# Performance work log

Hardware: AMD Instinct MI355X
Metric: run time of the kernel (lower is better)

## Reference

```python
import jax, jax.numpy as jnp
import numpy as np

BATCH = 65536
IN_DIM = 512
LATENT = 32
NUM_TRIL = LATENT * (LATENT + 1) // 2  # 528
# torch.tril_indices returns row-major order, same as np.tril_indices
_ROWS, _COLS = np.tril_indices(LATENT)
ROWS = jnp.asarray(_ROWS)
COLS = jnp.asarray(_COLS)
BN_EPS = 1e-5
LRELU_SLOPE = 0.01


def setup_inputs() -> dict:
    key = jax.random.key(0)
    ks = jax.random.split(key, 12)
    x = jax.random.normal(ks[0], (BATCH, IN_DIM), dtype=jnp.float32)
    s_enc = 1.0 / np.sqrt(IN_DIM)
    s_lat = 1.0 / np.sqrt(LATENT)
    return {
        "x": x,
        "W_enc": jax.random.uniform(ks[1], (IN_DIM, LATENT), minval=-s_enc, maxval=s_enc, dtype=jnp.float32),
        "b_enc": jax.random.uniform(ks[2], (LATENT,), minval=-s_enc, maxval=s_enc, dtype=jnp.float32),
        "bn_gamma": jnp.ones((LATENT,), dtype=jnp.float32),
        "bn_beta": jnp.zeros((LATENT,), dtype=jnp.float32),
        "bn_mean": 0.1 * jax.random.normal(ks[3], (LATENT,), dtype=jnp.float32),
        "bn_var": jax.random.uniform(ks[4], (LATENT,), minval=0.5, maxval=1.5, dtype=jnp.float32),
        "W_mu": jax.random.uniform(ks[5], (LATENT, LATENT), minval=-s_lat, maxval=s_lat, dtype=jnp.float32),
        "b_mu": jax.random.uniform(ks[6], (LATENT,), minval=-s_lat, maxval=s_lat, dtype=jnp.float32),
        "W_ch": jax.random.uniform(ks[7], (LATENT, NUM_TRIL), minval=-s_lat, maxval=s_lat, dtype=jnp.float32),
        "b_ch": jax.random.uniform(ks[8], (NUM_TRIL,), minval=-s_lat, maxval=s_lat, dtype=jnp.float32),
    }


def _leaky_relu(v):
    return jnp.where(v >= 0, v, LRELU_SLOPE * v)


def reference(x, W_enc, b_enc, bn_gamma, bn_beta, bn_mean, bn_var, W_mu, b_mu, W_ch, b_ch):
    # downsampled_enc: Linear(512, latent) -> BatchNorm1d (eval mode) -> LeakyReLU
    h = x @ W_enc + b_enc                                        # [B, L]
    h = bn_gamma * (h - bn_mean) * jax.lax.rsqrt(bn_var + BN_EPS) + bn_beta
    h = _leaky_relu(h)
    # mu head
    mus = _leaky_relu(h @ W_mu + b_mu)                           # [B, L]
    # log-cholesky head -> 528 lower-triangular elements
    elts = _leaky_relu(h @ W_ch + b_ch)                          # [B, 528]
    B = x.shape[0]
    L = jnp.zeros((B, LATENT, LATENT), dtype=jnp.float32)
    L = L.at[:, ROWS, COLS].set(elts)                            # scatter into lower triangle
    di = jnp.arange(LATENT)
    diag = L[:, di, di]
    diag = jnp.clip(jax.nn.softplus(diag), 0.001, 100.0) + 0.01
    L = L.at[:, di, di].set(diag)
    # cov = L L^T + 0.01 I
    cov = jnp.einsum('bij,bkj->bik', L, L) + 0.01 * jnp.eye(LATENT, dtype=jnp.float32)
    return (h, mus, cov)
```

## Files before the change

### kernel.cpp

```cpp
#include <hip/hip_runtime.h>
#include <math.h>

constexpr int BATCH  = 65536;
constexpr int IN_DIM = 512;
constexpr int LATENT = 32;
constexpr int NTRIL  = 528;
constexpr float BN_EPS = 1e-5f;
constexpr float SLOPE  = 0.01f;

constexpr int RPB  = 64;
constexpr int CROWS = 16;
constexpr int HSTR = 36;
constexpr int PSTR = 36;

constexpr int LPACK   = 576;
constexpr int LSTRIDE = 584;

__device__ __host__ __forceinline__ constexpr int rstart(int i) {
    const int g = i >> 2, r = i & 3;
    return 4 * (i + 2 * g * (g - 1) + r * g);
}

__device__ __forceinline__ float leaky(float v) {
    return v >= 0.0f ? v : SLOPE * v;
}

extern "C" __global__ __launch_bounds__(256, 4)
void enc_kernel(const float* __restrict__ x,
                const float* __restrict__ W_enc,
                const float* __restrict__ b_enc,
                const float* __restrict__ bn_gamma,
                const float* __restrict__ bn_beta,
                const float* __restrict__ bn_mean,
                const float* __restrict__ bn_var,
                float* __restrict__ h_out)
{
    __shared__ float part[4][RPB][PSTR];

    const int t = threadIdx.x;
    const int w = __builtin_amdgcn_readfirstlane(t >> 6);
    const int l = t & 63;
    const int row0 = blockIdx.x * RPB;

    {
        const float4* __restrict__ xp =
            (const float4*)(x + (size_t)(row0 + l) * IN_DIM + w * (IN_DIM / 4));
        const float* __restrict__ Wq = W_enc + (w * (IN_DIM / 4)) * LATENT;

        float acc[LATENT];
        #pragma unroll
        for (int c = 0; c < LATENT; ++c) acc[c] = 0.0f;

        float4 q0 = xp[0];
        float4 q1 = xp[1];
        #pragma unroll 2
        for (int k4 = 0; k4 < IN_DIM / 16; ++k4) {
            const float4 xv = q0;
            q0 = q1;
            const int pf = (k4 < IN_DIM / 16 - 2) ? (k4 + 2) : (IN_DIM / 16 - 1);
            q1 = xp[pf];

            const float* __restrict__ Wk = Wq + (4 * k4) * LATENT;
            #pragma unroll
            for (int c = 0; c < LATENT; ++c) acc[c] = fmaf(xv.x, Wk[c],            acc[c]);
            #pragma unroll
            for (int c = 0; c < LATENT; ++c) acc[c] = fmaf(xv.y, Wk[LATENT + c],   acc[c]);
            #pragma unroll
            for (int c = 0; c < LATENT; ++c) acc[c] = fmaf(xv.z, Wk[2*LATENT + c], acc[c]);
            #pragma unroll
            for (int c = 0; c < LATENT; ++c) acc[c] = fmaf(xv.w, Wk[3*LATENT + c], acc[c]);
        }

        #pragma unroll
        for (int c4 = 0; c4 < LATENT / 4; ++c4)
            *(float4*)&part[w][l][4 * c4] =
                make_float4(acc[4*c4+0], acc[4*c4+1], acc[4*c4+2], acc[4*c4+3]);
    }
    __syncthreads();

    {
        const int r  = t >> 2;
        const int c0 = (t & 3) * 8;
        float v[8];
        #pragma unroll
        for (int i = 0; i < 8; ++i) v[i] = 0.0f;
        #pragma unroll
        for (int ww = 0; ww < 4; ++ww) {
            const float4 p0 = *(const float4*)&part[ww][r][c0];
            const float4 p1 = *(const float4*)&part[ww][r][c0 + 4];
            v[0]+=p0.x; v[1]+=p0.y; v[2]+=p0.z; v[3]+=p0.w;
            v[4]+=p1.x; v[5]+=p1.y; v[6]+=p1.z; v[7]+=p1.w;
        }
        float hv[8];
        #pragma unroll
        for (int i = 0; i < 8; ++i) {
            const int c = c0 + i;
            float u = v[i] + b_enc[c];
            u = bn_gamma[c] * (u - bn_mean[c]) * rsqrtf(bn_var[c] + BN_EPS) + bn_beta[c];
            hv[i] = leaky(u);
        }
        float4* __restrict__ hp = (float4*)(h_out + (size_t)(row0 + r) * LATENT + c0);
        hp[0] = make_float4(hv[0], hv[1], hv[2], hv[3]);
        hp[1] = make_float4(hv[4], hv[5], hv[6], hv[7]);
    }
}

extern "C" __global__ __launch_bounds__(256)
void elts_kernel(const float* __restrict__ h_in,
                 const float* __restrict__ W_mu,
                 const float* __restrict__ b_mu,
                 const float* __restrict__ W_ch,
                 const float* __restrict__ b_ch,
                 float* __restrict__ mu_out,
                 float* __restrict__ cov_out)
{
    __shared__ float h_sh[RPB][HSTR];

    const int t = threadIdx.x;
    const int row0 = blockIdx.x * RPB;

    {
        const int r  = t >> 2;
        const int c0 = (t & 3) * 8;
        const float4* __restrict__ hg =
            (const float4*)(h_in + (size_t)(row0 + r) * LATENT + c0);
        const float4 a0 = hg[0];
        const float4 a1 = hg[1];
        *(float4*)&h_sh[r][c0]     = a0;
        *(float4*)&h_sh[r][c0 + 4] = a1;
    }
    __syncthreads();

    {
        const int c = t & 31;
        const int g = t >> 5;
        float wmu[LATENT];
        #pragma unroll
        for (int k = 0; k < LATENT; ++k) wmu[k] = W_mu[k * LATENT + c];
        const float bm = b_mu[c];
        #pragma unroll
        for (int j = 0; j < 8; ++j) {
            const int r = g * 8 + j;
            const float4* __restrict__ hr = (const float4*)&h_sh[r][0];
            float a = bm;
            #pragma unroll
            for (int k4 = 0; k4 < 8; ++k4) {
                const float4 hvv = hr[k4];
                a += hvv.x*wmu[4*k4+0] + hvv.y*wmu[4*k4+1]
                   + hvv.z*wmu[4*k4+2] + hvv.w*wmu[4*k4+3];
            }
            mu_out[(size_t)(row0 + r) * LATENT + c] = leaky(a);
        }
    }

    #pragma unroll 1
    for (int jid = t; jid < 132 * 16; jid += 256) {
        const int q  = jid % 132;
        const int rg = jid / 132;
        const int j0 = 4 * q;
        const int r0s = 4 * rg;

        float4 a0 = make_float4(b_ch[j0+0], b_ch[j0+1], b_ch[j0+2], b_ch[j0+3]);
        float4 a1 = a0, a2 = a0, a3 = a0;

        const float* __restrict__ wbase = W_ch + j0;
        #pragma unroll
        for (int kq = 0; kq < 8; ++kq) {
            const float4 w0 = *(const float4*)(wbase + (4*kq + 0) * NTRIL);
            const float4 w1 = *(const float4*)(wbase + (4*kq + 1) * NTRIL);
            const float4 w2 = *(const float4*)(wbase + (4*kq + 2) * NTRIL);
            const float4 w3 = *(const float4*)(wbase + (4*kq + 3) * NTRIL);
            const float4 h0 = *(const float4*)&h_sh[r0s + 0][4*kq];
            const float4 h1 = *(const float4*)&h_sh[r0s + 1][4*kq];
            const float4 h2 = *(const float4*)&h_sh[r0s + 2][4*kq];
            const float4 h3 = *(const float4*)&h_sh[r0s + 3][4*kq];
            a0.x += h0.x*w0.x + h0.y*w1.x + h0.z*w2.x + h0.w*w3.x;
            a0.y += h0.x*w0.y + h0.y*w1.y + h0.z*w2.y + h0.w*w3.y;
            a0.z += h0.x*w0.z + h0.y*w1.z + h0.z*w2.z + h0.w*w3.z;
            a0.w += h0.x*w0.w + h0.y*w1.w + h0.z*w2.w + h0.w*w3.w;
            a1.x += h1.x*w0.x + h1.y*w1.x + h1.z*w2.x + h1.w*w3.x;
            a1.y += h1.x*w0.y + h1.y*w1.y + h1.z*w2.y + h1.w*w3.y;
            a1.z += h1.x*w0.z + h1.y*w1.z + h1.z*w2.z + h1.w*w3.z;
            a1.w += h1.x*w0.w + h1.y*w1.w + h1.z*w2.w + h1.w*w3.w;
            a2.x += h2.x*w0.x + h2.y*w1.x + h2.z*w2.x + h2.w*w3.x;
            a2.y += h2.x*w0.y + h2.y*w1.y + h2.z*w2.y + h2.w*w3.y;
            a2.z += h2.x*w0.z + h2.y*w1.z + h2.z*w2.z + h2.w*w3.z;
            a2.w += h2.x*w0.w + h2.y*w1.w + h2.z*w2.w + h2.w*w3.w;
            a3.x += h3.x*w0.x + h3.y*w1.x + h3.z*w2.x + h3.w*w3.x;
            a3.y += h3.x*w0.y + h3.y*w1.y + h3.z*w2.y + h3.w*w3.y;
            a3.z += h3.x*w0.z + h3.y*w1.z + h3.z*w2.z + h3.w*w3.z;
            a3.w += h3.x*w0.w + h3.y*w1.w + h3.z*w2.w + h3.w*w3.w;
        }

        #pragma unroll
        for (int e = 0; e < 4; ++e) {
            const int j = j0 + e;
            int ri = (int)((sqrtf(8.0f * (float)j + 1.0f) - 1.0f) * 0.5f);
            if ((ri + 1) * (ri + 2) / 2 <= j) ++ri;
            if (ri * (ri + 1) / 2 > j) --ri;
            const int ci = j - ri * (ri + 1) / 2;
            const bool isdiag = (ci == ri);
            const int off = rstart(ri) + ci;

            #pragma unroll
            for (int rr = 0; rr < 4; ++rr) {
                float vv = (rr == 0) ? ((e==0)?a0.x:(e==1)?a0.y:(e==2)?a0.z:a0.w)
                         : (rr == 1) ? ((e==0)?a1.x:(e==1)?a1.y:(e==2)?a1.z:a1.w)
                         : (rr == 2) ? ((e==0)?a2.x:(e==1)?a2.y:(e==2)?a2.z:a2.w)
                                     : ((e==0)?a3.x:(e==1)?a3.y:(e==2)?a3.z:a3.w);
                vv = leaky(vv);
                if (isdiag) {
                    float sp = vv > 20.0f ? vv : log1pf(__expf(vv));
                    vv = fminf(fmaxf(sp, 0.001f), 100.0f) + 0.01f;
                }
                cov_out[(size_t)(row0 + r0s + rr) * (LATENT * LATENT) + off] = vv;
            }
        }
    }
}

extern "C" __global__ __launch_bounds__(256)
void cov_kernel(float* __restrict__ cov_out)
{
    __shared__ float L_sh[CROWS * LSTRIDE];

    const int t = threadIdx.x;
    const int row0b = blockIdx.x * CROWS;

    #pragma unroll 1
    for (int s = t; s < CROWS * (LPACK / 4); s += 256) {
        const int lr = s / (LPACK / 4);
        const int qi = s % (LPACK / 4);
        const float4 v = *(const float4*)
            (cov_out + (size_t)(row0b + lr) * (LATENT * LATENT) + 4 * qi);
        *(float4*)&L_sh[lr * LSTRIDE + 4 * qi] = v;
    }
    __syncthreads();

    #pragma unroll 1
    for (int s = t; s < CROWS * 48; s += 256) {
        const int lr  = s / 48;
        const int idx = s % 48;
        const int g  = idx / 6;
        const int wv = idx % 6;
        const int rig = (wv < 3) ? 0 : (wv < 5) ? 1 : 2;
        const int po  = (wv < 3) ? wv : (wv < 5) ? wv - 3 : 0;
        const int i   = 4 * g + rig;
        L_sh[lr * LSTRIDE + rstart(i) + (i + 1) + po] = 0.0f;
    }
    __syncthreads();

    {
        const int lr = t >> 4;
        const int p  = t & 15;
        const float* __restrict__ Lb = L_sh + lr * LSTRIDE;

        float li0[16];
        {
            const int s0 = rstart(p);
            #pragma unroll
            for (int qq = 0; qq < 4; ++qq) {
                const float4 v = *(const float4*)(Lb + s0 + 4*qq);
                li0[4*qq+0] = (4*qq+0 <= p) ? v.x : 0.0f;
                li0[4*qq+1] = (4*qq+1 <= p) ? v.y : 0.0f;
                li0[4*qq+2] = (4*qq+2 <= p) ? v.z : 0.0f;
                li0[4*qq+3] = (4*qq+3 <= p) ? v.w : 0.0f;
            }
        }
        float li1[32];
        {
            const int i1 = p + 16;
            const int s1 = rstart(i1);
            #pragma unroll
            for (int qq = 0; qq < 8; ++qq) {
                const float4 v = *(const float4*)(Lb + s1 + 4*qq);
                li1[4*qq+0] = (4*qq+0 <= i1) ? v.x : 0.0f;
                li1[4*qq+1] = (4*qq+1 <= i1) ? v.y : 0.0f;
                li1[4*qq+2] = (4*qq+2 <= i1) ? v.z : 0.0f;
                li1[4*qq+3] = (4*qq+3 <= i1) ? v.w : 0.0f;
            }
        }

        float* __restrict__ cov0 =
            cov_out + (size_t)(row0b + lr) * (LATENT * LATENT) + (size_t)p * LATENT;
        float* __restrict__ cov1 = cov0 + 16 * LATENT;

        float cr0[16], cr1[16];

        #pragma unroll
        for (int k = 0; k < 16; ++k) {
            const int qk = (k >> 2) + 1;
            const float* __restrict__ Lk = Lb + rstart(k);
            float d0 = 0.0f, d1 = 0.0f;
            #pragma unroll
            for (int qq = 0; qq < qk; ++qq) {
                const float4 wv = *(const float4*)(Lk + 4*qq);
                d0 += li0[4*qq+0]*wv.x + li0[4*qq+1]*wv.y
                    + li0[4*qq+2]*wv.z + li0[4*qq+3]*wv.w;
                d1 += li1[4*qq+0]*wv.x + li1[4*qq+1]*wv.y
                    + li1[4*qq+2]*wv.z + li1[4*qq+3]*wv.w;
            }
            cr0[k] = (k == p) ? d0 + 0.01f : d0;
            cr1[k] = d1;
        }
        #pragma unroll
        for (int k4 = 0; k4 < 4; ++k4) {
            *(float4*)(cov0 + 4*k4) = make_float4(cr0[4*k4], cr0[4*k4+1], cr0[4*k4+2], cr0[4*k4+3]);
            *(float4*)(cov1 + 4*k4) = make_float4(cr1[4*k4], cr1[4*k4+1], cr1[4*k4+2], cr1[4*k4+3]);
        }

        #pragma unroll
        for (int k = 16; k < 32; ++k) {
            const int qk = (k >> 2) + 1;
            const float* __restrict__ Lk = Lb + rstart(k);
            float d0 = 0.0f, d1 = 0.0f;
            #pragma unroll
            for (int qq = 0; qq < 4; ++qq) {
                const float4 wv = *(const float4*)(Lk + 4*qq);
                d0 += li0[4*qq+0]*wv.x + li0[4*qq+1]*wv.y
                    + li0[4*qq+2]*wv.z + li0[4*qq+3]*wv.w;
            }
            #pragma unroll
            for (int qq = 0; qq < 8; ++qq) {
                if (qq < qk) {
                    const float4 wv = *(const float4*)(Lk + 4*qq);
                    d1 += li1[4*qq+0]*wv.x + li1[4*qq+1]*wv.y
                        + li1[4*qq+2]*wv.z + li1[4*qq+3]*wv.w;
                }
            }
            cr0[k-16] = d0;
            cr1[k-16] = (k == p + 16) ? d1 + 0.01f : d1;
        }
        #pragma unroll
        for (int k4 = 0; k4 < 4; ++k4) {
            *(float4*)(cov0 + 16 + 4*k4) = make_float4(cr0[4*k4], cr0[4*k4+1], cr0[4*k4+2], cr0[4*k4+3]);
            *(float4*)(cov1 + 16 + 4*k4) = make_float4(cr1[4*k4], cr1[4*k4+1], cr1[4*k4+2], cr1[4*k4+3]);
        }
    }
}

extern "C" void kernel_launch(void* const* d_in, const int* in_sizes, int n_in,
                              void* d_out, int out_size, void* d_ws, size_t ws_size,
                              hipStream_t stream) {
    const float* x        = (const float*)d_in[0];
    const float* W_enc    = (const float*)d_in[1];
    const float* b_enc    = (const float*)d_in[2];
    const float* bn_gamma = (const float*)d_in[3];
    const float* bn_beta  = (const float*)d_in[4];
    const float* bn_mean  = (const float*)d_in[5];
    const float* bn_var   = (const float*)d_in[6];
    const float* W_mu     = (const float*)d_in[7];
    const float* b_mu     = (const float*)d_in[8];
    const float* W_ch     = (const float*)d_in[9];
    const float* b_ch     = (const float*)d_in[10];
    float* out = (float*)d_out;

    float* h_out   = out;
    float* mu_out  = out + (size_t)BATCH * LATENT;
    float* cov_out = out + (size_t)2 * BATCH * LATENT;

    enc_kernel<<<dim3(BATCH / RPB), dim3(256), 0, stream>>>(
        x, W_enc, b_enc, bn_gamma, bn_beta, bn_mean, bn_var, h_out);
    elts_kernel<<<dim3(BATCH / RPB), dim3(256), 0, stream>>>(
        h_out, W_mu, b_mu, W_ch, b_ch, mu_out, cov_out);
    cov_kernel<<<dim3(BATCH / CROWS), dim3(256), 0, stream>>>(cov_out);
}
```

Baseline: 807.1 us.

## Fuse Cholesky element and covariance kernels through shared-memory L tiles

The elts and cov kernels are merged into one decoder kernel. The packed lower-triangular L elements are now written to a zeroed shared-memory buffer in sub-blocks of 16 rows instead of going to global memory. The L L^T product is then computed straight from shared memory. This removes the global write and re-read of the packed L (about 2.3 KB per row), one kernel launch and the separate zeroing pass. In exchange it adds about 37 KB of shared memory per block plus extra barriers, which may limit occupancy. The triangular index decode is also made incremental instead of using a per-element sqrt.

```diff
diff --git a/kernel.cpp b/kernel.cpp
--- a/kernel.cpp
+++ b/kernel.cpp
@@ -9,11 +9,10 @@
 constexpr float SLOPE  = 0.01f;
 
 constexpr int RPB  = 64;
-constexpr int CROWS = 16;
+constexpr int SUBR = 16;
 constexpr int HSTR = 36;
 constexpr int PSTR = 36;
 
-constexpr int LPACK   = 576;
 constexpr int LSTRIDE = 584;
 
 __device__ __host__ __forceinline__ constexpr int rstart(int i) {
@@ -105,19 +104,27 @@
     }
 }
 
-extern "C" __global__ __launch_bounds__(256)
-void elts_kernel(const float* __restrict__ h_in,
-                 const float* __restrict__ W_mu,
-                 const float* __restrict__ b_mu,
-                 const float* __restrict__ W_ch,
-                 const float* __restrict__ b_ch,
-                 float* __restrict__ mu_out,
-                 float* __restrict__ cov_out)
+extern "C" __global__ __launch_bounds__(256, 4)
+void dec_kernel(const float* __restrict__ h_in,
+                const float* __restrict__ W_mu,
+                const float* __restrict__ b_mu,
+                const float* __restrict__ W_ch,
+                const float* __restrict__ b_ch,
+                float* __restrict__ mu_out,
+                float* __restrict__ cov_out)
 {
     __shared__ float h_sh[RPB][HSTR];
+    __shared__ float L_sh[SUBR * LSTRIDE];
 
     const int t = threadIdx.x;
     const int row0 = blockIdx.x * RPB;
+
+    {
+        float4* z4 = (float4*)L_sh;
+        const float4 z = make_float4(0.f, 0.f, 0.f, 0.f);
+        #pragma unroll 1
+        for (int s = t; s < SUBR * LSTRIDE / 4; s += 256) z4[s] = z;
+    }
 
     {
         const int r  = t >> 2;
@@ -154,188 +161,164 @@
     }
 
     #pragma unroll 1
-    for (int jid = t; jid < 132 * 16; jid += 256) {
-        const int q  = jid % 132;
-        const int rg = jid / 132;
-        const int j0 = 4 * q;
-        const int r0s = 4 * rg;
-
-        float4 a0 = make_float4(b_ch[j0+0], b_ch[j0+1], b_ch[j0+2], b_ch[j0+3]);
-        float4 a1 = a0, a2 = a0, a3 = a0;
-
-        const float* __restrict__ wbase = W_ch + j0;
-        #pragma unroll
-        for (int kq = 0; kq < 8; ++kq) {
-            const float4 w0 = *(const float4*)(wbase + (4*kq + 0) * NTRIL);
-            const float4 w1 = *(const float4*)(wbase + (4*kq + 1) * NTRIL);
-            const float4 w2 = *(const float4*)(wbase + (4*kq + 2) * NTRIL);
-            const float4 w3 = *(const float4*)(wbase + (4*kq + 3) * NTRIL);
-            const float4 h0 = *(const float4*)&h_sh[r0s + 0][4*kq];
-            const float4 h1 = *(const float4*)&h_sh[r0s + 1][4*kq];
-            const float4 h2 = *(const float4*)&h_sh[r0s + 2][4*kq];
-            const float4 h3 = *(const float4*)&h_sh[r0s + 3][4*kq];
-            a0.x += h0.x*w0.x + h0.y*w1.x + h0.z*w2.x + h0.w*w3.x;
-            a0.y += h0.x*w0.y + h0.y*w1.y + h0.z*w2.y + h0.w*w3.y;
-            a0.z += h0.x*w0.z + h0.y*w1.z + h0.z*w2.z + h0.w*w3.z;
-            a0.w += h0.x*w0.w + h0.y*w1.w + h0.z*w2.w + h0.w*w3.w;
-            a1.x += h1.x*w0.x + h1.y*w1.x + h1.z*w2.x + h1.w*w3.x;
-            a1.y += h1.x*w0.y + h1.y*w1.y + h1.z*w2.y + h1.w*w3.y;
-            a1.z += h1.x*w0.z + h1.y*w1.z + h1.z*w2.z + h1.w*w3.z;
-            a1.w += h1.x*w0.w + h1.y*w1.w + h1.z*w2.w + h1.w*w3.w;
-            a2.x += h2.x*w0.x + h2.y*w1.x + h2.z*w2.x + h2.w*w3.x;
-            a2.y += h2.x*w0.y + h2.y*w1.y + h2.z*w2.y + h2.w*w3.y;
-            a2.z += h2.x*w0.z + h2.y*w1.z + h2.z*w2.z + h2.w*w3.z;
-            a2.w += h2.x*w0.w + h2.y*w1.w + h2.z*w2.w + h2.w*w3.w;
-            a3.x += h3.x*w0.x + h3.y*w1.x + h3.z*w2.x + h3.w*w3.x;
-            a3.y += h3.x*w0.y + h3.y*w1.y + h3.z*w2.y + h3.w*w3.y;
-            a3.z += h3.x*w0.z + h3.y*w1.z + h3.z*w2.z + h3.w*w3.z;
-            a3.w += h3.x*w0.w + h3.y*w1.w + h3.z*w2.w + h3.w*w3.w;
-        }
-
-        #pragma unroll
-        for (int e = 0; e < 4; ++e) {
-            const int j = j0 + e;
-            int ri = (int)((sqrtf(8.0f * (float)j + 1.0f) - 1.0f) * 0.5f);
-            if ((ri + 1) * (ri + 2) / 2 <= j) ++ri;
-            if (ri * (ri + 1) / 2 > j) --ri;
-            const int ci = j - ri * (ri + 1) / 2;
-            const bool isdiag = (ci == ri);
-            const int off = rstart(ri) + ci;
-
-            #pragma unroll
-            for (int rr = 0; rr < 4; ++rr) {
-                float vv = (rr == 0) ? ((e==0)?a0.x:(e==1)?a0.y:(e==2)?a0.z:a0.w)
-                         : (rr == 1) ? ((e==0)?a1.x:(e==1)?a1.y:(e==2)?a1.z:a1.w)
-                         : (rr == 2) ? ((e==0)?a2.x:(e==1)?a2.y:(e==2)?a2.z:a2.w)
-                                     : ((e==0)?a3.x:(e==1)?a3.y:(e==2)?a3.z:a3.w);
-                vv = leaky(vv);
-                if (isdiag) {
-                    float sp = vv > 20.0f ? vv : log1pf(__expf(vv));
-                    vv = fminf(fmaxf(sp, 0.001f), 100.0f) + 0.01f;
-                }
-                cov_out[(size_t)(row0 + r0s + rr) * (LATENT * LATENT) + off] = vv;
-            }
-        }
-    }
-}
-
-extern "C" __global__ __launch_bounds__(256)
-void cov_kernel(float* __restrict__ cov_out)
-{
-    __shared__ float L_sh[CROWS * LSTRIDE];
-
-    const int t = threadIdx.x;
-    const int row0b = blockIdx.x * CROWS;
-
-    #pragma unroll 1
-    for (int s = t; s < CROWS * (LPACK / 4); s += 256) {
-        const int lr = s / (LPACK / 4);
-        const int qi = s % (LPACK / 4);
-        const float4 v = *(const float4*)
-            (cov_out + (size_t)(row0b + lr) * (LATENT * LATENT) + 4 * qi);
-        *(float4*)&L_sh[lr * LSTRIDE + 4 * qi] = v;
-    }
-    __syncthreads();
-
-    #pragma unroll 1
-    for (int s = t; s < CROWS * 48; s += 256) {
-        const int lr  = s / 48;
-        const int idx = s % 48;
-        const int g  = idx / 6;
-        const int wv = idx % 6;
-        const int rig = (wv < 3) ? 0 : (wv < 5) ? 1 : 2;
-        const int po  = (wv < 3) ? wv : (wv < 5) ? wv - 3 : 0;
-        const int i   = 4 * g + rig;
-        L_sh[lr * LSTRIDE + rstart(i) + (i + 1) + po] = 0.0f;
-    }
-    __syncthreads();
-
-    {
-        const int lr = t >> 4;
-        const int p  = t & 15;
-        const float* __restrict__ Lb = L_sh + lr * LSTRIDE;
-
-        float li0[16];
+    for (int sb = 0; sb < RPB / SUBR; ++sb) {
+        const int rbl = sb * SUBR;
+
+        #pragma unroll 1
+        for (int jid = t; jid < 132 * 4; jid += 256) {
+            const int q  = jid % 132;
+            const int rg = jid / 132;
+            const int j0 = 4 * q;
+            const int r0l = 4 * rg;
+            const int r0g = rbl + r0l;
+
+            float4 a0 = make_float4(b_ch[j0+0], b_ch[j0+1], b_ch[j0+2], b_ch[j0+3]);
+            float4 a1 = a0, a2 = a0, a3 = a0;
+
+            const float* __restrict__ wbase = W_ch + j0;
+            #pragma unroll
+            for (int kq = 0; kq < 8; ++kq) {
+                const float4 w0 = *(const float4*)(wbase + (4*kq + 0) * NTRIL);
+                const float4 w1 = *(const float4*)(wbase + (4*kq + 1) * NTRIL);
+                const float4 w2 = *(const float4*)(wbase + (4*kq + 2) * NTRIL);
+                const float4 w3 = *(const float4*)(wbase + (4*kq + 3) * NTRIL);
+                const float4 h0 = *(const float4*)&h_sh[r0g + 0][4*kq];
+                const float4 h1 = *(const float4*)&h_sh[r0g + 1][4*kq];
+                const float4 h2 = *(const float4*)&h_sh[r0g + 2][4*kq];
+                const float4 h3 = *(const float4*)&h_sh[r0g + 3][4*kq];
+                a0.x += h0.x*w0.x + h0.y*w1.x + h0.z*w2.x + h0.w*w3.x;
+                a0.y += h0.x*w0.y + h0.y*w1.y + h0.z*w2.y + h0.w*w3.y;
+                a0.z += h0.x*w0.z + h0.y*w1.z + h0.z*w2.z + h0.w*w3.z;
+                a0.w += h0.x*w0.w + h0.y*w1.w + h0.z*w2.w + h0.w*w3.w;
+                a1.x += h1.x*w0.x + h1.y*w1.x + h1.z*w2.x + h1.w*w3.x;
+                a1.y += h1.x*w0.y + h1.y*w1.y + h1.z*w2.y + h1.w*w3.y;
+                a1.z += h1.x*w0.z + h1.y*w1.z + h1.z*w2.z + h1.w*w3.z;
+                a1.w += h1.x*w0.w + h1.y*w1.w + h1.z*w2.w + h1.w*w3.w;
+                a2.x += h2.x*w0.x + h2.y*w1.x + h2.z*w2.x + h2.w*w3.x;
+                a2.y += h2.x*w0.y + h2.y*w1.y + h2.z*w2.y + h2.w*w3.y;
+                a2.z += h2.x*w0.z + h2.y*w1.z + h2.z*w2.z + h2.w*w3.z;
+                a2.w += h2.x*w0.w + h2.y*w1.w + h2.z*w2.w + h2.w*w3.w;
+                a3.x += h3.x*w0.x + h3.y*w1.x + h3.z*w2.x + h3.w*w3.x;
+                a3.y += h3.x*w0.y + h3.y*w1.y + h3.z*w2.y + h3.w*w3.y;
+                a3.z += h3.x*w0.z + h3.y*w1.z + h3.z*w2.z + h3.w*w3.z;
+                a3.w += h3.x*w0.w + h3.y*w1.w + h3.z*w2.w + h3.w*w3.w;
+            }
+
+            int ri = (int)((sqrtf(8.0f * (float)j0 + 1.0f) - 1.0f) * 0.5f);
+            if ((ri + 1) * (ri + 2) / 2 <= j0) ++ri;
+            if (ri * (ri + 1) / 2 > j0) --ri;
+            int ci = j0 - ri * (ri + 1) / 2;
+
+            #pragma unroll
+            for (int e = 0; e < 4; ++e) {
+                const bool isdiag = (ci == ri);
+                const int off = rstart(ri) + ci;
+                #pragma unroll
+                for (int rr = 0; rr < 4; ++rr) {
+                    float vv = (rr == 0) ? ((e==0)?a0.x:(e==1)?a0.y:(e==2)?a0.z:a0.w)
+                             : (rr == 1) ? ((e==0)?a1.x:(e==1)?a1.y:(e==2)?a1.z:a1.w)
+                             : (rr == 2) ? ((e==0)?a2.x:(e==1)?a2.y:(e==2)?a2.z:a2.w)
+                                         : ((e==0)?a3.x:(e==1)?a3.y:(e==2)?a3.z:a3.w);
+                    vv = leaky(vv);
+                    if (isdiag) {
+                        float sp = vv > 20.0f ? vv : log1pf(__expf(vv));
+                        vv = fminf(fmaxf(sp, 0.001f), 100.0f) + 0.01f;
+                    }
+                    L_sh[(r0l + rr) * LSTRIDE + off] = vv;
+                }
+                ++ci;
+                if (ci > ri) { ++ri; ci = 0; }
+            }
+        }
+        __syncthreads();
+
         {
-            const int s0 = rstart(p);
-            #pragma unroll
-            for (int qq = 0; qq < 4; ++qq) {
-                const float4 v = *(const float4*)(Lb + s0 + 4*qq);
-                li0[4*qq+0] = (4*qq+0 <= p) ? v.x : 0.0f;
-                li0[4*qq+1] = (4*qq+1 <= p) ? v.y : 0.0f;
-                li0[4*qq+2] = (4*qq+2 <= p) ? v.z : 0.0f;
-                li0[4*qq+3] = (4*qq+3 <= p) ? v.w : 0.0f;
-            }
-        }
-        float li1[32];
-        {
-            const int i1 = p + 16;
-            const int s1 = rstart(i1);
-            #pragma unroll
-            for (int qq = 0; qq < 8; ++qq) {
-                const float4 v = *(const float4*)(Lb + s1 + 4*qq);
-                li1[4*qq+0] = (4*qq+0 <= i1) ? v.x : 0.0f;
-                li1[4*qq+1] = (4*qq+1 <= i1) ? v.y : 0.0f;
-                li1[4*qq+2] = (4*qq+2 <= i1) ? v.z : 0.0f;
-                li1[4*qq+3] = (4*qq+3 <= i1) ? v.w : 0.0f;
-            }
-        }
-
-        float* __restrict__ cov0 =
-            cov_out + (size_t)(row0b + lr) * (LATENT * LATENT) + (size_t)p * LATENT;
-        float* __restrict__ cov1 = cov0 + 16 * LATENT;
-
-        float cr0[16], cr1[16];
-
-        #pragma unroll
-        for (int k = 0; k < 16; ++k) {
-            const int qk = (k >> 2) + 1;
-            const float* __restrict__ Lk = Lb + rstart(k);
-            float d0 = 0.0f, d1 = 0.0f;
-            #pragma unroll
-            for (int qq = 0; qq < qk; ++qq) {
-                const float4 wv = *(const float4*)(Lk + 4*qq);
-                d0 += li0[4*qq+0]*wv.x + li0[4*qq+1]*wv.y
-                    + li0[4*qq+2]*wv.z + li0[4*qq+3]*wv.w;
-                d1 += li1[4*qq+0]*wv.x + li1[4*qq+1]*wv.y
-                    + li1[4*qq+2]*wv.z + li1[4*qq+3]*wv.w;
-            }
-            cr0[k] = (k == p) ? d0 + 0.01f : d0;
-            cr1[k] = d1;
-        }
-        #pragma unroll
-        for (int k4 = 0; k4 < 4; ++k4) {
-            *(float4*)(cov0 + 4*k4) = make_float4(cr0[4*k4], cr0[4*k4+1], cr0[4*k4+2], cr0[4*k4+3]);
-            *(float4*)(cov1 + 4*k4) = make_float4(cr1[4*k4], cr1[4*k4+1], cr1[4*k4+2], cr1[4*k4+3]);
-        }
-
-        #pragma unroll
-        for (int k = 16; k < 32; ++k) {
-            const int qk = (k >> 2) + 1;
-            const float* __restrict__ Lk = Lb + rstart(k);
-            float d0 = 0.0f, d1 = 0.0f;
-            #pragma unroll
-            for (int qq = 0; qq < 4; ++qq) {
-                const float4 wv = *(const float4*)(Lk + 4*qq);
-                d0 += li0[4*qq+0]*wv.x + li0[4*qq+1]*wv.y
-                    + li0[4*qq+2]*wv.z + li0[4*qq+3]*wv.w;
-            }
-            #pragma unroll
-            for (int qq = 0; qq < 8; ++qq) {
-                if (qq < qk) {
+            const int lr = t >> 4;
+            const int p  = t & 15;
+            const float* __restrict__ Lb = L_sh + lr * LSTRIDE;
+
+            float li0[16];
+            {
+                const int s0 = rstart(p);
+                #pragma unroll
+                for (int qq = 0; qq < 4; ++qq) {
+                    const float4 v = *(const float4*)(Lb + s0 + 4*qq);
+                    li0[4*qq+0] = (4*qq+0 <= p) ? v.x : 0.0f;
+                    li0[4*qq+1] = (4*qq+1 <= p) ? v.y : 0.0f;
+                    li0[4*qq+2] = (4*qq+2 <= p) ? v.z : 0.0f;
+                    li0[4*qq+3] = (4*qq+3 <= p) ? v.w : 0.0f;
+                }
+            }
+            float li1[32];
+            {
+                const int i1 = p + 16;
+                const int s1 = rstart(i1);
+                #pragma unroll
+                for (int qq = 0; qq < 8; ++qq) {
+                    const float4 v = *(const float4*)(Lb + s1 + 4*qq);
+                    li1[4*qq+0] = (4*qq+0 <= i1) ? v.x : 0.0f;
+                    li1[4*qq+1] = (4*qq+1 <= i1) ? v.y : 0.0f;
+                    li1[4*qq+2] = (4*qq+2 <= i1) ? v.z : 0.0f;
+                    li1[4*qq+3] = (4*qq+3 <= i1) ? v.w : 0.0f;
+                }
+            }
+
+            const size_t grow = (size_t)(row0 + rbl + lr);
+            float* __restrict__ cov0 =
+                cov_out + grow * (size_t)(LATENT * LATENT) + (size_t)p * LATENT;
+            float* __restrict__ cov1 = cov0 + 16 * LATENT;
+
+            float cr0[16], cr1[16];
+
+            #pragma unroll
+            for (int k = 0; k < 16; ++k) {
+                const int qk = (k >> 2) + 1;
+                const float* __restrict__ Lk = Lb + rstart(k);
+                float d0 = 0.0f, d1 = 0.0f;
+                #pragma unroll
+                for (int qq = 0; qq < qk; ++qq) {
                     const float4 wv = *(const float4*)(Lk + 4*qq);
+                    d0 += li0[4*qq+0]*wv.x + li0[4*qq+1]*wv.y
+                        + li0[4*qq+2]*wv.z + li0[4*qq+3]*wv.w;
                     d1 += li1[4*qq+0]*wv.x + li1[4*qq+1]*wv.y
                         + li1[4*qq+2]*wv.z + li1[4*qq+3]*wv.w;
                 }
-            }
-            cr0[k-16] = d0;
-            cr1[k-16] = (k == p + 16) ? d1 + 0.01f : d1;
-        }
-        #pragma unroll
-        for (int k4 = 0; k4 < 4; ++k4) {
-            *(float4*)(cov0 + 16 + 4*k4) = make_float4(cr0[4*k4], cr0[4*k4+1], cr0[4*k4+2], cr0[4*k4+3]);
-            *(float4*)(cov1 + 16 + 4*k4) = make_float4(cr1[4*k4], cr1[4*k4+1], cr1[4*k4+2], cr1[4*k4+3]);
-        }
+                cr0[k] = (k == p) ? d0 + 0.01f : d0;
+                cr1[k] = d1;
+            }
+            #pragma unroll
+            for (int k4 = 0; k4 < 4; ++k4) {
+                *(float4*)(cov0 + 4*k4) = make_float4(cr0[4*k4], cr0[4*k4+1], cr0[4*k4+2], cr0[4*k4+3]);
+                *(float4*)(cov1 + 4*k4) = make_float4(cr1[4*k4], cr1[4*k4+1], cr1[4*k4+2], cr1[4*k4+3]);
+            }
+
+            #pragma unroll
+            for (int k = 16; k < 32; ++k) {
+                const int qk = (k >> 2) + 1;
+                const float* __restrict__ Lk = Lb + rstart(k);
+                float d0 = 0.0f, d1 = 0.0f;
+                #pragma unroll
+                for (int qq = 0; qq < 8; ++qq) {
+                    if (qq < qk) {
+                        const float4 wv = *(const float4*)(Lk + 4*qq);
+                        if (qq < 4) {
+                            d0 += li0[4*qq+0]*wv.x + li0[4*qq+1]*wv.y
+                                + li0[4*qq+2]*wv.z + li0[4*qq+3]*wv.w;
+                        }
+                        d1 += li1[4*qq+0]*wv.x + li1[4*qq+1]*wv.y
+                            + li1[4*qq+2]*wv.z + li1[4*qq+3]*wv.w;
+                    }
+                }
+                cr0[k-16] = d0;
+                cr1[k-16] = (k == p + 16) ? d1 + 0.01f : d1;
+            }
+            #pragma unroll
+            for (int k4 = 0; k4 < 4; ++k4) {
+                *(float4*)(cov0 + 16 + 4*k4) = make_float4(cr0[4*k4], cr0[4*k4+1], cr0[4*k4+2], cr0[4*k4+3]);
+                *(float4*)(cov1 + 16 + 4*k4) = make_float4(cr1[4*k4], cr1[4*k4+1], cr1[4*k4+2], cr1[4*k4+3]);
+            }
+        }
+        __syncthreads();
     }
 }
 
@@ -361,7 +344,6 @@
 
     enc_kernel<<<dim3(BATCH / RPB), dim3(256), 0, stream>>>(
         x, W_enc, b_enc, bn_gamma, bn_beta, bn_mean, bn_var, h_out);
-    elts_kernel<<<dim3(BATCH / RPB), dim3(256), 0, stream>>>(
+    dec_kernel<<<dim3(BATCH / RPB), dim3(256), 0, stream>>>(
         h_out, W_mu, b_mu, W_ch, b_ch, mu_out, cov_out);
-    cov_kernel<<<dim3(BATCH / CROWS), dim3(256), 0, stream>>>(cov_out);
-}
+}
```

Measured after the change: 771.6 us. 4.4% less time.
